# Performance work log

Measured on AMD Instinct MI355X. Metric: run time of the kernel, lower is better.

Reference implementation:

```python
import jax, jax.numpy as jnp
import numpy as np

N, E = 10000, 320000
NF, HF = 256, 256  # input_nf/output_nf, hidden_nf
EPS = 1e-8


def setup_inputs() -> dict:
    key = jax.random.key(0)
    ks = jax.random.split(key, 20)
    h = jax.random.normal(ks[0], (N, NF), jnp.float32)
    coord = jax.random.normal(ks[1], (N, 3), jnp.float32)
    edge_index = jax.random.randint(ks[2], (2, E), 0, N, jnp.int32)

    def dense(k, fan_in, fan_out, scale=None):
        s = scale if scale is not None else 1.0 / np.sqrt(fan_in)
        W = jax.random.normal(k, (fan_in, fan_out), jnp.float32) * s
        b = jnp.zeros((fan_out,), jnp.float32)
        return W, b

    We1, be1 = dense(ks[3], 2 * NF + 1, HF)   # edge_mlp layer 1
    We2, be2 = dense(ks[4], HF, HF)           # edge_mlp layer 2
    Wn1, bn1 = dense(ks[5], HF + NF, HF)      # node_mlp layer 1
    Wn2, bn2 = dense(ks[6], HF, NF)           # node_mlp layer 2
    Wc1, bc1 = dense(ks[7], HF, HF)           # coord_mlp layer 1
    Wc2, bc2 = dense(ks[8], HF, 1, scale=0.001)  # coord_mlp final, tiny init (xavier gain=0.001)
    return dict(h=h, coord=coord, edge_index=edge_index,
                We1=We1, be1=be1, We2=We2, be2=be2,
                Wn1=Wn1, bn1=bn1, Wn2=Wn2, bn2=bn2,
                Wc1=Wc1, bc1=bc1, Wc2=Wc2, bc2=bc2)


def _segment_sum(data, seg_ids, num_segments):
    return jax.ops.segment_sum(data, seg_ids, num_segments=num_segments)


def reference(h, coord, edge_index, We1, be1, We2, be2, Wn1, bn1, Wn2, bn2, Wc1, bc1, Wc2, bc2):
    row, col = edge_index[0], edge_index[1]

    # coord2radial
    coord_diff = coord[row] - coord[col]                    # [E, 3]
    radial = jnp.sum(coord_diff ** 2, axis=1, keepdims=True)  # [E, 1]

    # edge model: MLP on [h_i, h_j, ||x_i - x_j||^2]
    edge_in = jnp.concatenate([h[row], h[col], radial], axis=1)  # [E, 2*NF+1]
    e = jax.nn.silu(edge_in @ We1 + be1)
    edge_feat = jax.nn.silu(e @ We2 + be2)                  # [E, HF]

    # coord model: coord_diff * coord_mlp(edge_feat), mean-aggregated
    c = jax.nn.silu(edge_feat @ Wc1 + bc1)
    trans = coord_diff * (c @ Wc2 + bc2)                    # [E, 3]
    agg_c = _segment_sum(trans, row, coord.shape[0])
    count = _segment_sum(jnp.ones_like(trans), row, coord.shape[0])
    coord_out = coord + agg_c / jnp.clip(count, 1.0)

    # node model: sum-aggregate edge features, concat with h, MLP
    agg_h = _segment_sum(edge_feat, row, h.shape[0])        # [N, HF]
    node_in = jnp.concatenate([h, agg_h], axis=1)           # [N, HF+NF]
    n = jax.nn.silu(node_in @ Wn1 + bn1)
    h_out = n @ Wn2 + bn2                                   # [N, NF]

    return h_out, coord_out
```

## Files before the change

### kernel.cpp

```cpp
#include <hip/hip_runtime.h>
#include <hip/hip_bf16.h>

typedef __bf16 bf16;
typedef __attribute__((ext_vector_type(8))) __bf16 bf16x8;
typedef __attribute__((ext_vector_type(4))) float f32x4;

static_assert(sizeof(bf16x8) == 16, "bf16x8 must be 16B");

constexpr int N_NODES = 10000;
constexpr int N_EDGES = 320000;
constexpr int KPAD    = 264;

__device__ __forceinline__ float silu_f(float x) {
  return x * __builtin_amdgcn_rcpf(1.0f + __expf(-x));
}

__device__ __forceinline__ unsigned pk_bf16(float lo, float hi) {
  unsigned a = __float_as_uint(lo) + 0x8000u;
  unsigned b = __float_as_uint(hi) + 0x8000u;
  return __builtin_amdgcn_perm(b, a, 0x07060302u);
}

__device__ __forceinline__ void mfmaT2_k256(const bf16* __restrict__ WT, int wstride,
                                            const bf16* Albs, int r, int q, f32x4 acc[2][4]) {
  for (int k0 = 0; k0 < 256; k0 += 32) {
    bf16x8 a[2], b[4];
#pragma unroll
    for (int mi = 0; mi < 2; ++mi)
      a[mi] = *(const bf16x8*)(WT + (size_t)(16 * mi + r) * wstride + k0 + q * 8);
#pragma unroll
    for (int ni = 0; ni < 4; ++ni)
      b[ni] = *(const bf16x8*)(Albs + (16 * ni + r) * KPAD + k0 + q * 8);
#pragma unroll
    for (int mi = 0; mi < 2; ++mi)
#pragma unroll
      for (int ni = 0; ni < 4; ++ni)
        acc[mi][ni] = __builtin_amdgcn_mfma_f32_16x16x32_bf16(a[mi], b[ni], acc[mi][ni], 0, 0, 0);
  }
}

__global__ __launch_bounds__(256) void prep_kernel(
    const float* __restrict__ h, const float* __restrict__ We1, const float* __restrict__ We2,
    const float* __restrict__ Wn1, const float* __restrict__ Wn2, const float* __restrict__ Wc1,
    const int* __restrict__ eidx,
    bf16* __restrict__ Hb, bf16* __restrict__ We1T, bf16* __restrict__ Wn1T,
    bf16* __restrict__ We2T, bf16* __restrict__ Wn2T, bf16* __restrict__ Wc1T,
    int* __restrict__ hist) {
  int bid = blockIdx.x, tid = threadIdx.x;
  if (bid < 10000) { int i = bid * 256 + tid; Hb[i] = (bf16)h[i]; return; }
  if (bid >= 11792) {
    int e = (bid - 11792) * 256 + tid;
    if (e < N_EDGES) atomicAdd(&hist[eidx[e]], 1);
    return;
  }
  int t = (bid - 10000) * 256 + tid;
  if (t < 131072) { int k = t >> 8, j = t & 255; We1T[j * 512 + k] = (bf16)We1[k * 256 + j]; return; }
  t -= 131072;
  if (t < 131072) { int k = t >> 8, j = t & 255; Wn1T[j * 512 + k] = (bf16)Wn1[k * 256 + j]; return; }
  t -= 131072;
  if (t < 65536) { int k = t >> 8, j = t & 255; We2T[j * 256 + k] = (bf16)We2[k * 256 + j]; return; }
  t -= 65536;
  if (t < 65536) { int k = t >> 8, j = t & 255; Wn2T[j * 256 + k] = (bf16)Wn2[k * 256 + j]; return; }
  t -= 65536;
  if (t < 65536) { int k = t >> 8, j = t & 255; Wc1T[j * 256 + k] = (bf16)Wc1[k * 256 + j]; return; }
}

__global__ __launch_bounds__(256) void scan_kernel(const int* __restrict__ hist,
                                                   int* __restrict__ base, int* __restrict__ cursor) {
  __shared__ int partial[256];
  int t = threadIdx.x;
  int s = 0;
  for (int i = 0; i < 40; ++i) { int idx = t * 40 + i; if (idx < N_NODES) s += hist[idx]; }
  partial[t] = s;
  __syncthreads();
  for (int d = 1; d < 256; d <<= 1) {
    int v = (t >= d) ? partial[t - d] : 0;
    __syncthreads();
    partial[t] += v;
    __syncthreads();
  }
  int run = partial[t] - s;
  for (int i = 0; i < 40; ++i) {
    int idx = t * 40 + i;
    if (idx < N_NODES) { base[idx] = run; cursor[idx] = run; run += hist[idx]; }
  }
}

__global__ __launch_bounds__(256) void scatter_kernel(const int* __restrict__ eidx, int* __restrict__ cursor,
                                                      int* __restrict__ rs, int* __restrict__ cs) {
  int e = blockIdx.x * 256 + threadIdx.x;
  if (e < N_EDGES) {
    int r = eidx[e], c = eidx[N_EDGES + e];
    int p = atomicAdd(&cursor[r], 1);
    rs[p] = r; cs[p] = c;
  }
}

__global__ __launch_bounds__(256, 2) void gemm_pq(const bf16* __restrict__ Hb,
                                                  const bf16* __restrict__ We1T,
                                                  const float* __restrict__ be1,
                                                  bf16* __restrict__ P, bf16* __restrict__ Q) {
  int tid = threadIdx.x, w = tid >> 6, lane = tid & 63, r = lane & 15, q = lane >> 4;
  int m0 = blockIdx.x * 64;
  int koff = blockIdx.y ? 256 : 0;
  bf16* OUT = blockIdx.y ? Q : P;
  bool addb = (blockIdx.y == 0);
  f32x4 acc[4][4];
#pragma unroll
  for (int mi = 0; mi < 4; ++mi)
#pragma unroll
    for (int ni = 0; ni < 4; ++ni) acc[mi][ni] = (f32x4){0.f, 0.f, 0.f, 0.f};

  for (int k0 = 0; k0 < 256; k0 += 32) {
    bf16x8 a[4], b[4];
#pragma unroll
    for (int mi = 0; mi < 4; ++mi)
      a[mi] = *(const bf16x8*)(We1T + (size_t)(w * 64 + 16 * mi + r) * 512 + koff + k0 + q * 8);
#pragma unroll
    for (int ni = 0; ni < 4; ++ni) {
      int m = m0 + 16 * ni + r; if (m > N_NODES - 1) m = N_NODES - 1;
      b[ni] = *(const bf16x8*)(Hb + (size_t)m * 256 + k0 + q * 8);
    }
#pragma unroll
    for (int mi = 0; mi < 4; ++mi)
#pragma unroll
      for (int ni = 0; ni < 4; ++ni)
        acc[mi][ni] = __builtin_amdgcn_mfma_f32_16x16x32_bf16(a[mi], b[ni], acc[mi][ni], 0, 0, 0);
  }
#pragma unroll
  for (int mi = 0; mi < 4; ++mi) {
    int ch = w * 64 + 16 * mi + 4 * q;
    float4 bv = addb ? *(const float4*)(be1 + ch) : (float4){0.f, 0.f, 0.f, 0.f};
#pragma unroll
    for (int ni = 0; ni < 4; ++ni) {
      int m = m0 + 16 * ni + r;
      if (m < N_NODES) {
        uint2 o;
        o.x = pk_bf16(acc[mi][ni][0] + bv.x, acc[mi][ni][1] + bv.y);
        o.y = pk_bf16(acc[mi][ni][2] + bv.z, acc[mi][ni][3] + bv.w);
        *(uint2*)(OUT + (size_t)m * 256 + ch) = o;
      }
    }
  }
}

__global__ __launch_bounds__(512, 6) void edge_kernel(
    const float* __restrict__ coord, const int* __restrict__ rs, const int* __restrict__ cs,
    const float* __restrict__ We1,
    const float* __restrict__ be2, const float* __restrict__ bc1,
    const float* __restrict__ Wc2, const float* __restrict__ bc2,
    const bf16* __restrict__ P, const bf16* __restrict__ Q,
    const bf16* __restrict__ We2T, const bf16* __restrict__ Wc1T,
    float* __restrict__ agg_h, float* __restrict__ agg_c) {
  __shared__ __align__(16) bf16 buf[64 * KPAD];
  __shared__ int s_row[64], s_col[64];
  __shared__ float s_rad[64], s_cd[64][3], s_scal[64];
  __shared__ int s_rs[65];
  __shared__ int s_nrun;

  int tid = threadIdx.x;
  int e0 = blockIdx.x * 64;
  int w = tid >> 6, lane = tid & 63, r = lane & 15, q = lane >> 4;

  if (tid < 64) {
    int e = e0 + tid;
    int ri = rs[e], ci = cs[e];
    s_row[tid] = ri; s_col[tid] = ci;
    float dx = coord[3 * ri + 0] - coord[3 * ci + 0];
    float dy = coord[3 * ri + 1] - coord[3 * ci + 1];
    float dz = coord[3 * ri + 2] - coord[3 * ci + 2];
    s_cd[tid][0] = dx; s_cd[tid][1] = dy; s_cd[tid][2] = dz;
    s_rad[tid] = dx * dx + dy * dy + dz * dz;
    s_scal[tid] = 0.f;
  }
  __syncthreads();

  if (tid < 64) {
    bool bnd = (tid == 0) || (s_row[tid] != s_row[tid - 1]);
    unsigned long long m = __ballot(bnd);
    int rank = __popcll(m & ((1ull << tid) - 1ull));
    if (bnd) s_rs[rank] = tid;
    if (tid == 0) { int R = __popcll(m); s_nrun = R; s_rs[R] = 64; }
  }

  {
    int off = (tid & 31) * 8;
    int esub = tid >> 5;
    float4 wa = *(const float4*)(We1 + 512 * 256 + off);
    float4 wb = *(const float4*)(We1 + 512 * 256 + off + 4);
#pragma unroll
    for (int p = 0; p < 4; ++p) {
      int e = p * 16 + esub;
      int ri = s_row[e], ci = s_col[e];
      bf16x8 pv = *(const bf16x8*)(P + (size_t)ri * 256 + off);
      bf16x8 qv = *(const bf16x8*)(Q + (size_t)ci * 256 + off);
      float rad = s_rad[e];
      float f0 = silu_f((float)pv[0] + (float)qv[0] + rad * wa.x);
      float f1 = silu_f((float)pv[1] + (float)qv[1] + rad * wa.y);
      float f2 = silu_f((float)pv[2] + (float)qv[2] + rad * wa.z);
      float f3 = silu_f((float)pv[3] + (float)qv[3] + rad * wa.w);
      float f4 = silu_f((float)pv[4] + (float)qv[4] + rad * wb.x);
      float f5 = silu_f((float)pv[5] + (float)qv[5] + rad * wb.y);
      float f6 = silu_f((float)pv[6] + (float)qv[6] + rad * wb.z);
      float f7 = silu_f((float)pv[7] + (float)qv[7] + rad * wb.w);
      uint4 o;
      o.x = pk_bf16(f0, f1); o.y = pk_bf16(f2, f3);
      o.z = pk_bf16(f4, f5); o.w = pk_bf16(f6, f7);
      *(uint4*)(buf + e * KPAD + off) = o;
    }
  }
  __syncthreads();

  {
    f32x4 acc[2][4];
#pragma unroll
    for (int mi = 0; mi < 2; ++mi)
#pragma unroll
      for (int ni = 0; ni < 4; ++ni) acc[mi][ni] = (f32x4){0.f, 0.f, 0.f, 0.f};
    mfmaT2_k256(We2T + (size_t)(w * 32) * 256, 256, buf, r, q, acc);
    __syncthreads();
#pragma unroll
    for (int mi = 0; mi < 2; ++mi) {
      int ch = w * 32 + 16 * mi + 4 * q;
      float4 bv = *(const float4*)(be2 + ch);
#pragma unroll
      for (int ni = 0; ni < 4; ++ni) {
        int edge = 16 * ni + r;
        float f0 = silu_f(acc[mi][ni][0] + bv.x);
        float f1 = silu_f(acc[mi][ni][1] + bv.y);
        float f2 = silu_f(acc[mi][ni][2] + bv.z);
        float f3 = silu_f(acc[mi][ni][3] + bv.w);
        uint2 o; o.x = pk_bf16(f0, f1); o.y = pk_bf16(f2, f3);
        *(uint2*)(buf + edge * KPAD + ch) = o;
      }
    }
  }
  __syncthreads();

  f32x4 acc2[2][4];
#pragma unroll
  for (int mi = 0; mi < 2; ++mi)
#pragma unroll
    for (int ni = 0; ni < 4; ++ni) acc2[mi][ni] = (f32x4){0.f, 0.f, 0.f, 0.f};
  mfmaT2_k256(Wc1T + (size_t)(w * 32) * 256, 256, buf, r, q, acc2);

  {
    int col = tid & 255, start = tid >> 8;
    int R = s_nrun;
    for (int rr = start; rr < R; rr += 2) {
      int st = s_rs[rr], en = s_rs[rr + 1];
      float s = 0.f;
      for (int e = st; e < en; ++e) s += (float)buf[e * KPAD + col];
      atomicAdd(&agg_h[(size_t)s_row[st] * 256 + col], s);
    }
  }

  {
    float part[4] = {0.f, 0.f, 0.f, 0.f};
#pragma unroll
    for (int mi = 0; mi < 2; ++mi) {
      int ch = w * 32 + 16 * mi + 4 * q;
      float4 bv = *(const float4*)(bc1 + ch);
      float4 wv = *(const float4*)(Wc2 + ch);
#pragma unroll
      for (int ni = 0; ni < 4; ++ni) {
        float f0 = silu_f(acc2[mi][ni][0] + bv.x);
        float f1 = silu_f(acc2[mi][ni][1] + bv.y);
        float f2 = silu_f(acc2[mi][ni][2] + bv.z);
        float f3 = silu_f(acc2[mi][ni][3] + bv.w);
        part[ni] += f0 * wv.x + f1 * wv.y + f2 * wv.z + f3 * wv.w;
      }
    }
#pragma unroll
    for (int ni = 0; ni < 4; ++ni)
      atomicAdd(&s_scal[16 * ni + r], part[ni]);
  }
  __syncthreads();

  if (tid < 3) {
    int R = s_nrun;
    for (int rr = 0; rr < R; ++rr) {
      int st = s_rs[rr], en = s_rs[rr + 1];
      float s = 0.f;
      for (int e = st; e < en; ++e) s += s_cd[e][tid] * (s_scal[e] + bc2[0]);
      atomicAdd(&agg_c[3 * s_row[st] + tid], s);
    }
  }
}

__global__ __launch_bounds__(512, 6) void node_kernel(
    const bf16* __restrict__ Hb, const float* __restrict__ agg_h,
    const int* __restrict__ hist, const float* __restrict__ coord, const float* __restrict__ agg_c,
    const bf16* __restrict__ Wn1T, const bf16* __restrict__ Wn2T,
    const float* __restrict__ bn1, const float* __restrict__ bn2,
    float* __restrict__ h_out, float* __restrict__ coord_out) {
  __shared__ __align__(16) bf16 buf[64 * KPAD];
  int tid = threadIdx.x, w = tid >> 6, lane = tid & 63, r = lane & 15, q = lane >> 4;
  int m0 = blockIdx.x * 64;

  if (tid < 64) {
    int m = m0 + tid;
    if (m < N_NODES) {
      float c = (float)hist[m]; if (c < 1.f) c = 1.f;
      float inv = __builtin_amdgcn_rcpf(c);
      coord_out[3 * m + 0] = coord[3 * m + 0] + agg_c[3 * m + 0] * inv;
      coord_out[3 * m + 1] = coord[3 * m + 1] + agg_c[3 * m + 1] * inv;
      coord_out[3 * m + 2] = coord[3 * m + 2] + agg_c[3 * m + 2] * inv;
    }
  }

  f32x4 acc[2][4];
#pragma unroll
  for (int mi = 0; mi < 2; ++mi)
#pragma unroll
    for (int ni = 0; ni < 4; ++ni) acc[mi][ni] = (f32x4){0.f, 0.f, 0.f, 0.f};
  const bf16* BT1 = Wn1T + (size_t)(w * 32) * 512;
  for (int k0 = 0; k0 < 256; k0 += 32) {
    bf16x8 a[2], b[4];
#pragma unroll
    for (int mi = 0; mi < 2; ++mi)
      a[mi] = *(const bf16x8*)(BT1 + (size_t)(16 * mi + r) * 512 + k0 + q * 8);
#pragma unroll
    for (int ni = 0; ni < 4; ++ni) {
      int m = m0 + 16 * ni + r; if (m > N_NODES - 1) m = N_NODES - 1;
      b[ni] = *(const bf16x8*)(Hb + (size_t)m * 256 + k0 + q * 8);
    }
#pragma unroll
    for (int mi = 0; mi < 2; ++mi)
#pragma unroll
      for (int ni = 0; ni < 4; ++ni)
        acc[mi][ni] = __builtin_amdgcn_mfma_f32_16x16x32_bf16(a[mi], b[ni], acc[mi][ni], 0, 0, 0);
  }
  for (int k0 = 0; k0 < 256; k0 += 32) {
    bf16x8 a[2], b[4];
#pragma unroll
    for (int mi = 0; mi < 2; ++mi)
      a[mi] = *(const bf16x8*)(BT1 + (size_t)(16 * mi + r) * 512 + 256 + k0 + q * 8);
#pragma unroll
    for (int ni = 0; ni < 4; ++ni) {
      int m = m0 + 16 * ni + r; if (m > N_NODES - 1) m = N_NODES - 1;
      const float* ap = agg_h + (size_t)m * 256 + k0 + q * 8;
      float4 u = *(const float4*)ap;
      float4 v = *(const float4*)(ap + 4);
      uint4 o;
      o.x = pk_bf16(u.x, u.y); o.y = pk_bf16(u.z, u.w);
      o.z = pk_bf16(v.x, v.y); o.w = pk_bf16(v.z, v.w);
      b[ni] = *(const bf16x8*)&o;
    }
#pragma unroll
    for (int mi = 0; mi < 2; ++mi)
#pragma unroll
      for (int ni = 0; ni < 4; ++ni)
        acc[mi][ni] = __builtin_amdgcn_mfma_f32_16x16x32_bf16(a[mi], b[ni], acc[mi][ni], 0, 0, 0);
  }
  __syncthreads();
#pragma unroll
  for (int mi = 0; mi < 2; ++mi) {
    int ch = w * 32 + 16 * mi + 4 * q;
    float4 bv = *(const float4*)(bn1 + ch);
#pragma unroll
    for (int ni = 0; ni < 4; ++ni) {
      int lm = 16 * ni + r;
      float f0 = silu_f(acc[mi][ni][0] + bv.x);
      float f1 = silu_f(acc[mi][ni][1] + bv.y);
      float f2 = silu_f(acc[mi][ni][2] + bv.z);
      float f3 = silu_f(acc[mi][ni][3] + bv.w);
      uint2 o; o.x = pk_bf16(f0, f1); o.y = pk_bf16(f2, f3);
      *(uint2*)(buf + lm * KPAD + ch) = o;
    }
  }
  __syncthreads();
  f32x4 acc2[2][4];
#pragma unroll
  for (int mi = 0; mi < 2; ++mi)
#pragma unroll
    for (int ni = 0; ni < 4; ++ni) acc2[mi][ni] = (f32x4){0.f, 0.f, 0.f, 0.f};
  mfmaT2_k256(Wn2T + (size_t)(w * 32) * 256, 256, buf, r, q, acc2);
#pragma unroll
  for (int mi = 0; mi < 2; ++mi) {
    int ch = w * 32 + 16 * mi + 4 * q;
    float4 bv = *(const float4*)(bn2 + ch);
#pragma unroll
    for (int ni = 0; ni < 4; ++ni) {
      int m = m0 + 16 * ni + r;
      if (m < N_NODES) {
        float4 o;
        o.x = acc2[mi][ni][0] + bv.x;
        o.y = acc2[mi][ni][1] + bv.y;
        o.z = acc2[mi][ni][2] + bv.z;
        o.w = acc2[mi][ni][3] + bv.w;
        *(float4*)(h_out + (size_t)m * 256 + ch) = o;
      }
    }
  }
}

extern "C" void kernel_launch(void* const* d_in, const int* in_sizes, int n_in,
                              void* d_out, int out_size, void* d_ws, size_t ws_size,
                              hipStream_t stream) {
  const float* h     = (const float*)d_in[0];
  const float* coord = (const float*)d_in[1];
  const int*   eidx  = (const int*)d_in[2];
  const float* We1 = (const float*)d_in[3];
  const float* be1 = (const float*)d_in[4];
  const float* We2 = (const float*)d_in[5];
  const float* be2 = (const float*)d_in[6];
  const float* Wn1 = (const float*)d_in[7];
  const float* bn1 = (const float*)d_in[8];
  const float* Wn2 = (const float*)d_in[9];
  const float* bn2 = (const float*)d_in[10];
  const float* Wc1 = (const float*)d_in[11];
  const float* bc1 = (const float*)d_in[12];
  const float* Wc2 = (const float*)d_in[13];
  const float* bc2 = (const float*)d_in[14];

  char* ws = (char*)d_ws;
  float* agg_h = (float*)(ws + 0);
  float* agg_c = (float*)(ws + 10240000);
  int*   hist  = (int*)  (ws + 10360000);
  int*   base  = (int*)  (ws + 10400000);
  int*   cursor= (int*)  (ws + 10440000);
  int*   rs    = (int*)  (ws + 10480000);
  int*   cs    = (int*)  (ws + 11760000);
  bf16* Hb   = (bf16*)(ws + 13040000);
  bf16* P    = (bf16*)(ws + 18160000);
  bf16* Q    = (bf16*)(ws + 23280000);
  bf16* We1T = (bf16*)(ws + 28400000);
  bf16* Wn1T = (bf16*)(ws + 28662144);
  bf16* We2T = (bf16*)(ws + 28924288);
  bf16* Wn2T = (bf16*)(ws + 29055360);
  bf16* Wc1T = (bf16*)(ws + 29186432);

  float* h_out = (float*)d_out;
  float* coord_out = h_out + (size_t)N_NODES * 256;

  hipMemsetAsync(ws, 0, 10400000, stream);
  prep_kernel<<<13042, 256, 0, stream>>>(h, We1, We2, Wn1, Wn2, Wc1, eidx,
                                         Hb, We1T, Wn1T, We2T, Wn2T, Wc1T, hist);
  scan_kernel<<<1, 256, 0, stream>>>(hist, base, cursor);
  scatter_kernel<<<1250, 256, 0, stream>>>(eidx, cursor, rs, cs);
  gemm_pq<<<dim3(157, 2), 256, 0, stream>>>(Hb, We1T, be1, P, Q);
  edge_kernel<<<5000, 512, 0, stream>>>(coord, rs, cs, We1, be2, bc1, Wc2, bc2,
                                        P, Q, We2T, Wc1T, agg_h, agg_c);
  node_kernel<<<157, 512, 0, stream>>>(Hb, agg_h, hist, coord, agg_c,
                                       Wn1T, Wn2T, bn1, bn2, h_out, coord_out);
}
```

Before: 482.8 us.

## Process four edge tiles per block with double-buffered P/Q gather prefetch

The edge kernel now handles 256 edges per block as four 64-edge tiles. Each tile's gathered P/Q rows for layer 1 are prefetched into registers while the current tile's MFMAs run, and written into a second LDS buffer. Segment boundaries are now a ballot bitmask, so the per-column run reductions become unrolled bitmask-driven loops instead of run-list loops. This amortizes setup and hides gather latency, but it doubles LDS use, lowers the occupancy hint to 4 and launches a quarter as many blocks.

```diff
diff --git a/kernel.cpp b/kernel.cpp
--- a/kernel.cpp
+++ b/kernel.cpp
@@ -10,6 +10,7 @@
 constexpr int N_NODES = 10000;
 constexpr int N_EDGES = 320000;
 constexpr int KPAD    = 264;
+constexpr int T_TILES = 4;
 
 __device__ __forceinline__ float silu_f(float x) {
   return x * __builtin_amdgcn_rcpf(1.0f + __expf(-x));
@@ -144,7 +145,7 @@
   }
 }
 
-__global__ __launch_bounds__(512, 6) void edge_kernel(
+__global__ __launch_bounds__(512, 4) void edge_kernel(
     const float* __restrict__ coord, const int* __restrict__ rs, const int* __restrict__ cs,
     const float* __restrict__ We1,
     const float* __restrict__ be2, const float* __restrict__ bc1,
@@ -152,49 +153,48 @@
     const bf16* __restrict__ P, const bf16* __restrict__ Q,
     const bf16* __restrict__ We2T, const bf16* __restrict__ Wc1T,
     float* __restrict__ agg_h, float* __restrict__ agg_c) {
-  __shared__ __align__(16) bf16 buf[64 * KPAD];
-  __shared__ int s_row[64], s_col[64];
-  __shared__ float s_rad[64], s_cd[64][3], s_scal[64];
-  __shared__ int s_rs[65];
-  __shared__ int s_nrun;
+  __shared__ __align__(16) bf16 bufE[2][64 * KPAD];
+  __shared__ int s_rowm[256], s_colm[256];
+  __shared__ float s_radm[256], s_cdm[256][3];
+  __shared__ float s_scal[2][64];
+  __shared__ unsigned long long s_bmask[T_TILES];
 
   int tid = threadIdx.x;
-  int e0 = blockIdx.x * 64;
+  int e0 = blockIdx.x * 256;
   int w = tid >> 6, lane = tid & 63, r = lane & 15, q = lane >> 4;
-
-  if (tid < 64) {
+  int off = (tid & 31) * 8;
+  int esub = tid >> 5;
+
+  if (tid < 256) {
     int e = e0 + tid;
     int ri = rs[e], ci = cs[e];
-    s_row[tid] = ri; s_col[tid] = ci;
+    s_rowm[tid] = ri; s_colm[tid] = ci;
     float dx = coord[3 * ri + 0] - coord[3 * ci + 0];
     float dy = coord[3 * ri + 1] - coord[3 * ci + 1];
     float dz = coord[3 * ri + 2] - coord[3 * ci + 2];
-    s_cd[tid][0] = dx; s_cd[tid][1] = dy; s_cd[tid][2] = dz;
-    s_rad[tid] = dx * dx + dy * dy + dz * dz;
-    s_scal[tid] = 0.f;
-  }
+    s_cdm[tid][0] = dx; s_cdm[tid][1] = dy; s_cdm[tid][2] = dz;
+    s_radm[tid] = dx * dx + dy * dy + dz * dz;
+  }
+  if (tid >= 256 && tid < 384) ((float*)s_scal)[tid - 256] = 0.f;
   __syncthreads();
-
-  if (tid < 64) {
-    bool bnd = (tid == 0) || (s_row[tid] != s_row[tid - 1]);
-    unsigned long long m = __ballot(bnd);
-    int rank = __popcll(m & ((1ull << tid) - 1ull));
-    if (bnd) s_rs[rank] = tid;
-    if (tid == 0) { int R = __popcll(m); s_nrun = R; s_rs[R] = 64; }
-  }
+  if (w < T_TILES) {
+    int e = w * 64 + lane;
+    bool bnd = (lane < 63) && (s_rowm[e] != s_rowm[e + 1]);
+    unsigned long long m = __ballot(bnd) | (1ull << 63);
+    if (lane == 0) s_bmask[w] = m;
+  }
+
+  float4 wa = *(const float4*)(We1 + 512 * 256 + off);
+  float4 wb = *(const float4*)(We1 + 512 * 256 + off + 4);
+  float bc2v = bc2[0];
 
   {
-    int off = (tid & 31) * 8;
-    int esub = tid >> 5;
-    float4 wa = *(const float4*)(We1 + 512 * 256 + off);
-    float4 wb = *(const float4*)(We1 + 512 * 256 + off + 4);
 #pragma unroll
     for (int p = 0; p < 4; ++p) {
       int e = p * 16 + esub;
-      int ri = s_row[e], ci = s_col[e];
-      bf16x8 pv = *(const bf16x8*)(P + (size_t)ri * 256 + off);
-      bf16x8 qv = *(const bf16x8*)(Q + (size_t)ci * 256 + off);
-      float rad = s_rad[e];
+      bf16x8 pv = *(const bf16x8*)(P + (size_t)s_rowm[e] * 256 + off);
+      bf16x8 qv = *(const bf16x8*)(Q + (size_t)s_colm[e] * 256 + off);
+      float rad = s_radm[e];
       float f0 = silu_f((float)pv[0] + (float)qv[0] + rad * wa.x);
       float f1 = silu_f((float)pv[1] + (float)qv[1] + rad * wa.y);
       float f2 = silu_f((float)pv[2] + (float)qv[2] + rad * wa.z);
@@ -206,19 +206,33 @@
       uint4 o;
       o.x = pk_bf16(f0, f1); o.y = pk_bf16(f2, f3);
       o.z = pk_bf16(f4, f5); o.w = pk_bf16(f6, f7);
-      *(uint4*)(buf + e * KPAD + off) = o;
+      *(uint4*)(&bufE[0][0] + e * KPAD + off) = o;
     }
   }
   __syncthreads();
 
-  {
+  int curb = 0;
+  for (int t = 0; t < T_TILES; ++t) {
+    int nxtb = curb ^ 1;
+
+    bf16x8 gp[4], gq[4];
+    if (t + 1 < T_TILES) {
+#pragma unroll
+      for (int p = 0; p < 4; ++p) {
+        int e = (t + 1) * 64 + p * 16 + esub;
+        gp[p] = *(const bf16x8*)(P + (size_t)s_rowm[e] * 256 + off);
+        gq[p] = *(const bf16x8*)(Q + (size_t)s_colm[e] * 256 + off);
+      }
+    }
+
     f32x4 acc[2][4];
 #pragma unroll
     for (int mi = 0; mi < 2; ++mi)
 #pragma unroll
       for (int ni = 0; ni < 4; ++ni) acc[mi][ni] = (f32x4){0.f, 0.f, 0.f, 0.f};
-    mfmaT2_k256(We2T + (size_t)(w * 32) * 256, 256, buf, r, q, acc);
+    mfmaT2_k256(We2T + (size_t)(w * 32) * 256, 256, &bufE[curb][0], r, q, acc);
     __syncthreads();
+
 #pragma unroll
     for (int mi = 0; mi < 2; ++mi) {
       int ch = w * 32 + 16 * mi + 4 * q;
@@ -231,60 +245,94 @@
         float f2 = silu_f(acc[mi][ni][2] + bv.z);
         float f3 = silu_f(acc[mi][ni][3] + bv.w);
         uint2 o; o.x = pk_bf16(f0, f1); o.y = pk_bf16(f2, f3);
-        *(uint2*)(buf + edge * KPAD + ch) = o;
-      }
-    }
-  }
-  __syncthreads();
-
-  f32x4 acc2[2][4];
-#pragma unroll
-  for (int mi = 0; mi < 2; ++mi)
-#pragma unroll
-    for (int ni = 0; ni < 4; ++ni) acc2[mi][ni] = (f32x4){0.f, 0.f, 0.f, 0.f};
-  mfmaT2_k256(Wc1T + (size_t)(w * 32) * 256, 256, buf, r, q, acc2);
-
-  {
-    int col = tid & 255, start = tid >> 8;
-    int R = s_nrun;
-    for (int rr = start; rr < R; rr += 2) {
-      int st = s_rs[rr], en = s_rs[rr + 1];
+        *(uint2*)(&bufE[curb][0] + edge * KPAD + ch) = o;
+      }
+    }
+
+    if (t + 1 < T_TILES) {
+#pragma unroll
+      for (int p = 0; p < 4; ++p) {
+        int e = (t + 1) * 64 + p * 16 + esub;
+        int el = p * 16 + esub;
+        float rad = s_radm[e];
+        float f0 = silu_f((float)gp[p][0] + (float)gq[p][0] + rad * wa.x);
+        float f1 = silu_f((float)gp[p][1] + (float)gq[p][1] + rad * wa.y);
+        float f2 = silu_f((float)gp[p][2] + (float)gq[p][2] + rad * wa.z);
+        float f3 = silu_f((float)gp[p][3] + (float)gq[p][3] + rad * wa.w);
+        float f4 = silu_f((float)gp[p][4] + (float)gq[p][4] + rad * wb.x);
+        float f5 = silu_f((float)gp[p][5] + (float)gq[p][5] + rad * wb.y);
+        float f6 = silu_f((float)gp[p][6] + (float)gq[p][6] + rad * wb.z);
+        float f7 = silu_f((float)gp[p][7] + (float)gq[p][7] + rad * wb.w);
+        uint4 o;
+        o.x = pk_bf16(f0, f1); o.y = pk_bf16(f2, f3);
+        o.z = pk_bf16(f4, f5); o.w = pk_bf16(f6, f7);
+        *(uint4*)(&bufE[nxtb][0] + el * KPAD + off) = o;
+      }
+      if (tid < 64) s_scal[nxtb][tid] = 0.f;
+    }
+    __syncthreads();
+
+    f32x4 acc2[2][4];
+#pragma unroll
+    for (int mi = 0; mi < 2; ++mi)
+#pragma unroll
+      for (int ni = 0; ni < 4; ++ni) acc2[mi][ni] = (f32x4){0.f, 0.f, 0.f, 0.f};
+    mfmaT2_k256(Wc1T + (size_t)(w * 32) * 256, 256, &bufE[curb][0], r, q, acc2);
+
+    {
+      int col = tid & 255, half = tid >> 8;
+      int ebase = half * 32;
+      unsigned bm = (unsigned)(s_bmask[t] >> ebase) | 0x80000000u;
+      const bf16* colp = &bufE[curb][0] + col;
+      float v[32];
+#pragma unroll
+      for (int i = 0; i < 32; ++i) v[i] = (float)colp[(ebase + i) * KPAD];
       float s = 0.f;
-      for (int e = st; e < en; ++e) s += (float)buf[e * KPAD + col];
-      atomicAdd(&agg_h[(size_t)s_row[st] * 256 + col], s);
-    }
-  }
-
-  {
-    float part[4] = {0.f, 0.f, 0.f, 0.f};
-#pragma unroll
-    for (int mi = 0; mi < 2; ++mi) {
-      int ch = w * 32 + 16 * mi + 4 * q;
-      float4 bv = *(const float4*)(bc1 + ch);
-      float4 wv = *(const float4*)(Wc2 + ch);
-#pragma unroll
-      for (int ni = 0; ni < 4; ++ni) {
-        float f0 = silu_f(acc2[mi][ni][0] + bv.x);
-        float f1 = silu_f(acc2[mi][ni][1] + bv.y);
-        float f2 = silu_f(acc2[mi][ni][2] + bv.z);
-        float f3 = silu_f(acc2[mi][ni][3] + bv.w);
-        part[ni] += f0 * wv.x + f1 * wv.y + f2 * wv.z + f3 * wv.w;
-      }
-    }
-#pragma unroll
-    for (int ni = 0; ni < 4; ++ni)
-      atomicAdd(&s_scal[16 * ni + r], part[ni]);
-  }
-  __syncthreads();
-
-  if (tid < 3) {
-    int R = s_nrun;
-    for (int rr = 0; rr < R; ++rr) {
-      int st = s_rs[rr], en = s_rs[rr + 1];
+#pragma unroll
+      for (int i = 0; i < 32; ++i) {
+        s += v[i];
+        if ((bm >> i) & 1u) {
+          atomicAdd(&agg_h[(size_t)s_rowm[t * 64 + ebase + i] * 256 + col], s);
+          s = 0.f;
+        }
+      }
+    }
+
+    {
+      float part[4] = {0.f, 0.f, 0.f, 0.f};
+#pragma unroll
+      for (int mi = 0; mi < 2; ++mi) {
+        int ch = w * 32 + 16 * mi + 4 * q;
+        float4 bv = *(const float4*)(bc1 + ch);
+        float4 wv = *(const float4*)(Wc2 + ch);
+#pragma unroll
+        for (int ni = 0; ni < 4; ++ni) {
+          float f0 = silu_f(acc2[mi][ni][0] + bv.x);
+          float f1 = silu_f(acc2[mi][ni][1] + bv.y);
+          float f2 = silu_f(acc2[mi][ni][2] + bv.z);
+          float f3 = silu_f(acc2[mi][ni][3] + bv.w);
+          part[ni] += f0 * wv.x + f1 * wv.y + f2 * wv.z + f3 * wv.w;
+        }
+      }
+#pragma unroll
+      for (int ni = 0; ni < 4; ++ni)
+        atomicAdd(&s_scal[curb][16 * ni + r], part[ni]);
+    }
+    __syncthreads();
+
+    if (tid < 3) {
       float s = 0.f;
-      for (int e = st; e < en; ++e) s += s_cd[e][tid] * (s_scal[e] + bc2[0]);
-      atomicAdd(&agg_c[3 * s_row[st] + tid], s);
-    }
+      unsigned long long bm = s_bmask[t];
+#pragma unroll 8
+      for (int e = 0; e < 64; ++e) {
+        s += s_cdm[t * 64 + e][tid] * (s_scal[curb][e] + bc2v);
+        if ((bm >> e) & 1ull) {
+          atomicAdd(&agg_c[3 * s_rowm[t * 64 + e] + tid], s);
+          s = 0.f;
+        }
+      }
+    }
+    curb = nxtb;
   }
 }
 
@@ -440,7 +488,7 @@
   scan_kernel<<<1, 256, 0, stream>>>(hist, base, cursor);
   scatter_kernel<<<1250, 256, 0, stream>>>(eidx, cursor, rs, cs);
   gemm_pq<<<dim3(157, 2), 256, 0, stream>>>(Hb, We1T, be1, P, Q);
-  edge_kernel<<<5000, 512, 0, stream>>>(coord, rs, cs, We1, be2, bc1, Wc2, bc2,
+  edge_kernel<<<1250, 512, 0, stream>>>(coord, rs, cs, We1, be2, bc1, Wc2, bc2,
                                         P, Q, We2T, Wc1T, agg_h, agg_c);
   node_kernel<<<157, 512, 0, stream>>>(Hb, agg_h, hist, coord, agg_c,
                                        Wn1T, Wn2T, bn1, bn2, h_out, coord_out);
```

Result: slower. 687.2 us (+42.3%).

## Halve edge tile to 32 with bitmask segment reduction, retile node kernel to 4 waves

Applied to the files above, without the earlier changes.

The edge kernel now handles 32 edges per block instead of 64, doubles the grid, raises the occupancy hint to 8 blocks, and replaces the run-start table with a boundary bitmask scanned inline for the agg_h and agg_c atomics. This is meant to cut LDS and register use so more waves stay resident and latency is hidden better. The cost is that every block reloads the We2T and Wc1T weight tiles for half as many edges, and more atomics are issued where runs cross tile edges. The node kernel moves to 256 threads with 4x4 accumulators per wave, so each wave covers 64 output channels.

```diff
diff --git a/kernel.cpp b/kernel.cpp
--- a/kernel.cpp
+++ b/kernel.cpp
@@ -10,6 +10,7 @@
 constexpr int N_NODES = 10000;
 constexpr int N_EDGES = 320000;
 constexpr int KPAD    = 264;
+constexpr int TILE    = 32;
 
 __device__ __forceinline__ float silu_f(float x) {
   return x * __builtin_amdgcn_rcpf(1.0f + __expf(-x));
@@ -21,18 +22,18 @@
   return __builtin_amdgcn_perm(b, a, 0x07060302u);
 }
 
-__device__ __forceinline__ void mfmaT2_k256(const bf16* __restrict__ WT, int wstride,
-                                            const bf16* Albs, int r, int q, f32x4 acc[2][4]) {
-  for (int k0 = 0; k0 < 256; k0 += 32) {
-    bf16x8 a[2], b[4];
-#pragma unroll
-    for (int mi = 0; mi < 2; ++mi)
-      a[mi] = *(const bf16x8*)(WT + (size_t)(16 * mi + r) * wstride + k0 + q * 8);
+__device__ __forceinline__ void mfmaT_k256(const bf16* __restrict__ WT, int wstride,
+                                           const bf16* Albs, int w, int r, int q, f32x4 acc[4][4]) {
+  for (int k0 = 0; k0 < 256; k0 += 32) {
+    bf16x8 a[4], b[4];
+#pragma unroll
+    for (int mi = 0; mi < 4; ++mi)
+      a[mi] = *(const bf16x8*)(WT + (size_t)(w * 64 + 16 * mi + r) * wstride + k0 + q * 8);
 #pragma unroll
     for (int ni = 0; ni < 4; ++ni)
       b[ni] = *(const bf16x8*)(Albs + (16 * ni + r) * KPAD + k0 + q * 8);
 #pragma unroll
-    for (int mi = 0; mi < 2; ++mi)
+    for (int mi = 0; mi < 4; ++mi)
 #pragma unroll
       for (int ni = 0; ni < 4; ++ni)
         acc[mi][ni] = __builtin_amdgcn_mfma_f32_16x16x32_bf16(a[mi], b[ni], acc[mi][ni], 0, 0, 0);
@@ -144,7 +145,7 @@
   }
 }
 
-__global__ __launch_bounds__(512, 6) void edge_kernel(
+__global__ __launch_bounds__(512, 8) void edge_kernel(
     const float* __restrict__ coord, const int* __restrict__ rs, const int* __restrict__ cs,
     const float* __restrict__ We1,
     const float* __restrict__ be2, const float* __restrict__ bc1,
@@ -152,17 +153,18 @@
     const bf16* __restrict__ P, const bf16* __restrict__ Q,
     const bf16* __restrict__ We2T, const bf16* __restrict__ Wc1T,
     float* __restrict__ agg_h, float* __restrict__ agg_c) {
-  __shared__ __align__(16) bf16 buf[64 * KPAD];
-  __shared__ int s_row[64], s_col[64];
-  __shared__ float s_rad[64], s_cd[64][3], s_scal[64];
-  __shared__ int s_rs[65];
-  __shared__ int s_nrun;
+  __shared__ __align__(16) bf16 buf[TILE * KPAD];
+  __shared__ int s_row[TILE], s_col[TILE];
+  __shared__ float s_rad[TILE], s_cd[TILE][3], s_scal[TILE];
+  __shared__ unsigned s_bmask;
 
   int tid = threadIdx.x;
-  int e0 = blockIdx.x * 64;
+  int e0 = blockIdx.x * TILE;
   int w = tid >> 6, lane = tid & 63, r = lane & 15, q = lane >> 4;
-
-  if (tid < 64) {
+  int off = (tid & 31) * 8;
+  int esub = tid >> 5;
+
+  if (tid < TILE) {
     int e = e0 + tid;
     int ri = rs[e], ci = cs[e];
     s_row[tid] = ri; s_col[tid] = ci;
@@ -175,25 +177,20 @@
   }
   __syncthreads();
 
-  if (tid < 64) {
-    bool bnd = (tid == 0) || (s_row[tid] != s_row[tid - 1]);
+  if (w == 0) {
+    bool bnd = (lane < TILE - 1) && (s_row[lane] != s_row[lane + 1]);
     unsigned long long m = __ballot(bnd);
-    int rank = __popcll(m & ((1ull << tid) - 1ull));
-    if (bnd) s_rs[rank] = tid;
-    if (tid == 0) { int R = __popcll(m); s_nrun = R; s_rs[R] = 64; }
+    if (lane == 0) s_bmask = (unsigned)m;
   }
 
   {
-    int off = (tid & 31) * 8;
-    int esub = tid >> 5;
     float4 wa = *(const float4*)(We1 + 512 * 256 + off);
     float4 wb = *(const float4*)(We1 + 512 * 256 + off + 4);
 #pragma unroll
-    for (int p = 0; p < 4; ++p) {
+    for (int p = 0; p < 2; ++p) {
       int e = p * 16 + esub;
-      int ri = s_row[e], ci = s_col[e];
-      bf16x8 pv = *(const bf16x8*)(P + (size_t)ri * 256 + off);
-      bf16x8 qv = *(const bf16x8*)(Q + (size_t)ci * 256 + off);
+      bf16x8 pv = *(const bf16x8*)(P + (size_t)s_row[e] * 256 + off);
+      bf16x8 qv = *(const bf16x8*)(Q + (size_t)s_col[e] * 256 + off);
       float rad = s_rad[e];
       float f0 = silu_f((float)pv[0] + (float)qv[0] + rad * wa.x);
       float f1 = silu_f((float)pv[1] + (float)qv[1] + rad * wa.y);
@@ -211,59 +208,88 @@
   }
   __syncthreads();
 
+  f32x4 acc[2][2];
+#pragma unroll
+  for (int mi = 0; mi < 2; ++mi)
+#pragma unroll
+    for (int ni = 0; ni < 2; ++ni) acc[mi][ni] = (f32x4){0.f, 0.f, 0.f, 0.f};
+  for (int k0 = 0; k0 < 256; k0 += 32) {
+    bf16x8 a[2], b[2];
+#pragma unroll
+    for (int mi = 0; mi < 2; ++mi)
+      a[mi] = *(const bf16x8*)(We2T + (size_t)(w * 32 + 16 * mi + r) * 256 + k0 + q * 8);
+#pragma unroll
+    for (int ni = 0; ni < 2; ++ni)
+      b[ni] = *(const bf16x8*)(buf + (16 * ni + r) * KPAD + k0 + q * 8);
+#pragma unroll
+    for (int mi = 0; mi < 2; ++mi)
+#pragma unroll
+      for (int ni = 0; ni < 2; ++ni)
+        acc[mi][ni] = __builtin_amdgcn_mfma_f32_16x16x32_bf16(a[mi], b[ni], acc[mi][ni], 0, 0, 0);
+  }
+  __syncthreads();
+
+#pragma unroll
+  for (int mi = 0; mi < 2; ++mi) {
+    int ch = w * 32 + 16 * mi + 4 * q;
+    float4 bv = *(const float4*)(be2 + ch);
+#pragma unroll
+    for (int ni = 0; ni < 2; ++ni) {
+      int edge = 16 * ni + r;
+      float f0 = silu_f(acc[mi][ni][0] + bv.x);
+      float f1 = silu_f(acc[mi][ni][1] + bv.y);
+      float f2 = silu_f(acc[mi][ni][2] + bv.z);
+      float f3 = silu_f(acc[mi][ni][3] + bv.w);
+      uint2 o; o.x = pk_bf16(f0, f1); o.y = pk_bf16(f2, f3);
+      *(uint2*)(buf + edge * KPAD + ch) = o;
+    }
+  }
+  __syncthreads();
+
+  f32x4 acc2[2][2];
+#pragma unroll
+  for (int mi = 0; mi < 2; ++mi)
+#pragma unroll
+    for (int ni = 0; ni < 2; ++ni) acc2[mi][ni] = (f32x4){0.f, 0.f, 0.f, 0.f};
+  for (int k0 = 0; k0 < 256; k0 += 32) {
+    bf16x8 a[2], b[2];
+#pragma unroll
+    for (int mi = 0; mi < 2; ++mi)
+      a[mi] = *(const bf16x8*)(Wc1T + (size_t)(w * 32 + 16 * mi + r) * 256 + k0 + q * 8);
+#pragma unroll
+    for (int ni = 0; ni < 2; ++ni)
+      b[ni] = *(const bf16x8*)(buf + (16 * ni + r) * KPAD + k0 + q * 8);
+#pragma unroll
+    for (int mi = 0; mi < 2; ++mi)
+#pragma unroll
+      for (int ni = 0; ni < 2; ++ni)
+        acc2[mi][ni] = __builtin_amdgcn_mfma_f32_16x16x32_bf16(a[mi], b[ni], acc2[mi][ni], 0, 0, 0);
+  }
+
   {
-    f32x4 acc[2][4];
-#pragma unroll
-    for (int mi = 0; mi < 2; ++mi)
-#pragma unroll
-      for (int ni = 0; ni < 4; ++ni) acc[mi][ni] = (f32x4){0.f, 0.f, 0.f, 0.f};
-    mfmaT2_k256(We2T + (size_t)(w * 32) * 256, 256, buf, r, q, acc);
-    __syncthreads();
-#pragma unroll
-    for (int mi = 0; mi < 2; ++mi) {
-      int ch = w * 32 + 16 * mi + 4 * q;
-      float4 bv = *(const float4*)(be2 + ch);
-#pragma unroll
-      for (int ni = 0; ni < 4; ++ni) {
-        int edge = 16 * ni + r;
-        float f0 = silu_f(acc[mi][ni][0] + bv.x);
-        float f1 = silu_f(acc[mi][ni][1] + bv.y);
-        float f2 = silu_f(acc[mi][ni][2] + bv.z);
-        float f3 = silu_f(acc[mi][ni][3] + bv.w);
-        uint2 o; o.x = pk_bf16(f0, f1); o.y = pk_bf16(f2, f3);
-        *(uint2*)(buf + edge * KPAD + ch) = o;
+    int col = tid & 255, half = tid >> 8;
+    int ebase = half * 16;
+    unsigned bm = ((s_bmask >> ebase) & 0xFFFFu) | 0x8000u;
+    float s = 0.f;
+#pragma unroll
+    for (int i = 0; i < 16; ++i) {
+      s += (float)buf[(ebase + i) * KPAD + col];
+      if ((bm >> i) & 1u) {
+        atomicAdd(&agg_h[(size_t)s_row[ebase + i] * 256 + col], s);
+        s = 0.f;
       }
     }
   }
-  __syncthreads();
-
-  f32x4 acc2[2][4];
-#pragma unroll
-  for (int mi = 0; mi < 2; ++mi)
-#pragma unroll
-    for (int ni = 0; ni < 4; ++ni) acc2[mi][ni] = (f32x4){0.f, 0.f, 0.f, 0.f};
-  mfmaT2_k256(Wc1T + (size_t)(w * 32) * 256, 256, buf, r, q, acc2);
 
   {
-    int col = tid & 255, start = tid >> 8;
-    int R = s_nrun;
-    for (int rr = start; rr < R; rr += 2) {
-      int st = s_rs[rr], en = s_rs[rr + 1];
-      float s = 0.f;
-      for (int e = st; e < en; ++e) s += (float)buf[e * KPAD + col];
-      atomicAdd(&agg_h[(size_t)s_row[st] * 256 + col], s);
-    }
-  }
-
-  {
-    float part[4] = {0.f, 0.f, 0.f, 0.f};
+    float part[2] = {0.f, 0.f};
 #pragma unroll
     for (int mi = 0; mi < 2; ++mi) {
       int ch = w * 32 + 16 * mi + 4 * q;
       float4 bv = *(const float4*)(bc1 + ch);
       float4 wv = *(const float4*)(Wc2 + ch);
 #pragma unroll
-      for (int ni = 0; ni < 4; ++ni) {
+      for (int ni = 0; ni < 2; ++ni) {
         float f0 = silu_f(acc2[mi][ni][0] + bv.x);
         float f1 = silu_f(acc2[mi][ni][1] + bv.y);
         float f2 = silu_f(acc2[mi][ni][2] + bv.z);
@@ -272,23 +298,27 @@
       }
     }
 #pragma unroll
-    for (int ni = 0; ni < 4; ++ni)
+    for (int ni = 0; ni < 2; ++ni)
       atomicAdd(&s_scal[16 * ni + r], part[ni]);
   }
   __syncthreads();
 
   if (tid < 3) {
-    int R = s_nrun;
-    for (int rr = 0; rr < R; ++rr) {
-      int st = s_rs[rr], en = s_rs[rr + 1];
-      float s = 0.f;
-      for (int e = st; e < en; ++e) s += s_cd[e][tid] * (s_scal[e] + bc2[0]);
-      atomicAdd(&agg_c[3 * s_row[st] + tid], s);
-    }
-  }
-}
-
-__global__ __launch_bounds__(512, 6) void node_kernel(
+    float bc2v = bc2[0];
+    unsigned bm = s_bmask | (1u << (TILE - 1));
+    float s = 0.f;
+#pragma unroll 8
+    for (int e = 0; e < TILE; ++e) {
+      s += s_cd[e][tid] * (s_scal[e] + bc2v);
+      if ((bm >> e) & 1u) {
+        atomicAdd(&agg_c[3 * s_row[e] + tid], s);
+        s = 0.f;
+      }
+    }
+  }
+}
+
+__global__ __launch_bounds__(256, 2) void node_kernel(
     const bf16* __restrict__ Hb, const float* __restrict__ agg_h,
     const int* __restrict__ hist, const float* __restrict__ coord, const float* __restrict__ agg_c,
     const bf16* __restrict__ Wn1T, const bf16* __restrict__ Wn2T,
@@ -309,33 +339,32 @@
     }
   }
 
-  f32x4 acc[2][4];
-#pragma unroll
-  for (int mi = 0; mi < 2; ++mi)
+  f32x4 acc[4][4];
+#pragma unroll
+  for (int mi = 0; mi < 4; ++mi)
 #pragma unroll
     for (int ni = 0; ni < 4; ++ni) acc[mi][ni] = (f32x4){0.f, 0.f, 0.f, 0.f};
-  const bf16* BT1 = Wn1T + (size_t)(w * 32) * 512;
-  for (int k0 = 0; k0 < 256; k0 += 32) {
-    bf16x8 a[2], b[4];
-#pragma unroll
-    for (int mi = 0; mi < 2; ++mi)
-      a[mi] = *(const bf16x8*)(BT1 + (size_t)(16 * mi + r) * 512 + k0 + q * 8);
+  for (int k0 = 0; k0 < 256; k0 += 32) {
+    bf16x8 a[4], b[4];
+#pragma unroll
+    for (int mi = 0; mi < 4; ++mi)
+      a[mi] = *(const bf16x8*)(Wn1T + (size_t)(w * 64 + 16 * mi + r) * 512 + k0 + q * 8);
 #pragma unroll
     for (int ni = 0; ni < 4; ++ni) {
       int m = m0 + 16 * ni + r; if (m > N_NODES - 1) m = N_NODES - 1;
       b[ni] = *(const bf16x8*)(Hb + (size_t)m * 256 + k0 + q * 8);
     }
 #pragma unroll
-    for (int mi = 0; mi < 2; ++mi)
+    for (int mi = 0; mi < 4; ++mi)
 #pragma unroll
       for (int ni = 0; ni < 4; ++ni)
         acc[mi][ni] = __builtin_amdgcn_mfma_f32_16x16x32_bf16(a[mi], b[ni], acc[mi][ni], 0, 0, 0);
   }
   for (int k0 = 0; k0 < 256; k0 += 32) {
-    bf16x8 a[2], b[4];
-#pragma unroll
-    for (int mi = 0; mi < 2; ++mi)
-      a[mi] = *(const bf16x8*)(BT1 + (size_t)(16 * mi + r) * 512 + 256 + k0 + q * 8);
+    bf16x8 a[4], b[4];
+#pragma unroll
+    for (int mi = 0; mi < 4; ++mi)
+      a[mi] = *(const bf16x8*)(Wn1T + (size_t)(w * 64 + 16 * mi + r) * 512 + 256 + k0 + q * 8);
 #pragma unroll
     for (int ni = 0; ni < 4; ++ni) {
       int m = m0 + 16 * ni + r; if (m > N_NODES - 1) m = N_NODES - 1;
@@ -348,15 +377,15 @@
       b[ni] = *(const bf16x8*)&o;
     }
 #pragma unroll
-    for (int mi = 0; mi < 2; ++mi)
+    for (int mi = 0; mi < 4; ++mi)
 #pragma unroll
       for (int ni = 0; ni < 4; ++ni)
         acc[mi][ni] = __builtin_amdgcn_mfma_f32_16x16x32_bf16(a[mi], b[ni], acc[mi][ni], 0, 0, 0);
   }
   __syncthreads();
 #pragma unroll
-  for (int mi = 0; mi < 2; ++mi) {
-    int ch = w * 32 + 16 * mi + 4 * q;
+  for (int mi = 0; mi < 4; ++mi) {
+    int ch = w * 64 + 16 * mi + 4 * q;
     float4 bv = *(const float4*)(bn1 + ch);
 #pragma unroll
     for (int ni = 0; ni < 4; ++ni) {
@@ -370,15 +399,15 @@
     }
   }
   __syncthreads();
-  f32x4 acc2[2][4];
-#pragma unroll
-  for (int mi = 0; mi < 2; ++mi)
+  f32x4 acc2[4][4];
+#pragma unroll
+  for (int mi = 0; mi < 4; ++mi)
 #pragma unroll
     for (int ni = 0; ni < 4; ++ni) acc2[mi][ni] = (f32x4){0.f, 0.f, 0.f, 0.f};
-  mfmaT2_k256(Wn2T + (size_t)(w * 32) * 256, 256, buf, r, q, acc2);
-#pragma unroll
-  for (int mi = 0; mi < 2; ++mi) {
-    int ch = w * 32 + 16 * mi + 4 * q;
+  mfmaT_k256(Wn2T, 256, buf, w, r, q, acc2);
+#pragma unroll
+  for (int mi = 0; mi < 4; ++mi) {
+    int ch = w * 64 + 16 * mi + 4 * q;
     float4 bv = *(const float4*)(bn2 + ch);
 #pragma unroll
     for (int ni = 0; ni < 4; ++ni) {
@@ -440,8 +469,8 @@
   scan_kernel<<<1, 256, 0, stream>>>(hist, base, cursor);
   scatter_kernel<<<1250, 256, 0, stream>>>(eidx, cursor, rs, cs);
   gemm_pq<<<dim3(157, 2), 256, 0, stream>>>(Hb, We1T, be1, P, Q);
-  edge_kernel<<<5000, 512, 0, stream>>>(coord, rs, cs, We1, be2, bc1, Wc2, bc2,
-                                        P, Q, We2T, Wc1T, agg_h, agg_c);
-  node_kernel<<<157, 512, 0, stream>>>(Hb, agg_h, hist, coord, agg_c,
+  edge_kernel<<<10000, 512, 0, stream>>>(coord, rs, cs, We1, be2, bc1, Wc2, bc2,
+                                         P, Q, We2T, Wc1T, agg_h, agg_c);
+  node_kernel<<<157, 256, 0, stream>>>(Hb, agg_h, hist, coord, agg_c,
                                        Wn1T, Wn2T, bn1, bn2, h_out, coord_out);
 }
```

Result: slower. 547.2 us (+13.3%).
